# Kernel tuning notes

Hardware: AMD Instinct MI355X
Metric: run time of the kernel (lower is better)

## Reference

```python
import jax, jax.numpy as jnp
import numpy as np

D = 100  # input_size


def _gru_scan(x, h0, wi, wh, bi, bh):
    # x: [B,T,Din], h0: [B,H], wi: [3H,Din], wh: [3H,H]  (PyTorch r,z,n gate order)
    xw = jnp.einsum('btd,gd->btg', x, wi) + bi  # [B,T,3H]
    def step(h, xt):
        gh = h @ wh.T + bh
        xr, xz, xn = jnp.split(xt, 3, axis=-1)
        hr, hz, hn = jnp.split(gh, 3, axis=-1)
        r = jax.nn.sigmoid(xr + hr)
        z = jax.nn.sigmoid(xz + hz)
        n = jnp.tanh(xn + r * hn)
        hn2 = (1 - z) * n + z * h
        return hn2, hn2
    _, ys = jax.lax.scan(step, h0, jnp.swapaxes(xw, 0, 1))
    return jnp.swapaxes(ys, 0, 1)  # [B,T,H]


def _bigru(x, wi, wh, bi, bh):
    B = x.shape[0]
    H = wh.shape[-1]
    h0 = jnp.zeros((B, H), x.dtype)
    f = _gru_scan(x, h0, wi[0], wh[0], bi[0], bh[0])
    b = _gru_scan(x[:, ::-1], h0, wi[1], wh[1], bi[1], bh[1])[:, ::-1]
    return jnp.concatenate([f, b], axis=-1)


def _gru_cell(x, h, wi, wh, bi, bh):
    gx = x @ wi.T + bi
    gh = h @ wh.T + bh
    xr, xz, xn = jnp.split(gx, 3, axis=-1)
    hr, hz, hn = jnp.split(gh, 3, axis=-1)
    r = jax.nn.sigmoid(xr + hr)
    z = jax.nn.sigmoid(xz + hz)
    n = jnp.tanh(xn + r * hn)
    return (1 - z) * n + z * h


def setup_inputs() -> dict:
    key = jax.random.key(0)
    ks = iter(jax.random.split(key, 40))
    def n(shape, s=0.08):
        return (jax.random.normal(next(ks), shape) * s).astype(jnp.float32)
    B, T, L, V = 32, 512, 64, 400000
    inp = {
        'x_word': jax.random.randint(next(ks), (B, T), 0, V),
        'x_query': jax.random.randint(next(ks), (B, L), 0, V),
        'embed': n((V, D), 0.3),
        'ctx_wi': n((2, 3 * D, D)), 'ctx_wh': n((2, 3 * D, D)),
        'ctx_bi': n((2, 3 * D)), 'ctx_bh': n((2, 3 * D)),
        'mod0_wi': n((2, 3 * D, 8 * D)), 'mod0_wh': n((2, 3 * D, D)),
        'mod0_bi': n((2, 3 * D)), 'mod0_bh': n((2, 3 * D)),
        'mod1_wi': n((2, 3 * D, 2 * D)), 'mod1_wh': n((2, 3 * D, D)),
        'mod1_bi': n((2, 3 * D)), 'mod1_bh': n((2, 3 * D)),
        'w_sim': n((6 * D,)),
        'enc_wi': n((12 * D, 2 * D)), 'enc_wh': n((12 * D, 4 * D)),
        'enc_bi': n((12 * D,)), 'enc_bh': n((12 * D,)),
        'dec_wi': n((12 * D, 2 * D)), 'dec_wh': n((12 * D, 4 * D)),
        'dec_bi': n((12 * D,)), 'dec_bh': n((12 * D,)),
        'w1': n((2 * D, 4 * D)), 'w2': n((2 * D, 4 * D)), 'vt': n((2 * D,)),
    }
    return inp


def reference(x_word, x_query, embed, ctx_wi, ctx_wh, ctx_bi, ctx_bh,
              mod0_wi, mod0_wh, mod0_bi, mod0_bh, mod1_wi, mod1_wh, mod1_bi, mod1_bh,
              w_sim, enc_wi, enc_wh, enc_bi, enc_bh, dec_wi, dec_wh, dec_bi, dec_bh,
              w1, w2, vt):
    B, T = x_word.shape
    # shared bidirectional context encoder over both context and query
    h = _bigru(embed[x_word], ctx_wi, ctx_wh, ctx_bi, ctx_bh)   # [B,T,2D]
    u = _bigru(embed[x_query], ctx_wi, ctx_wh, ctx_bi, ctx_bh)  # [B,L,2D]
    # trilinear similarity W @ cat(h,u,h*u), fused (no [B,T,L,6D] materialization)
    w1s, w2s, w3s = jnp.split(w_sim, 3)
    S = (jnp.einsum('btd,d->bt', h, w1s)[:, :, None]
         + jnp.einsum('bld,d->bl', u, w2s)[:, None, :]
         + jnp.einsum('btd,bld->btl', h * w3s, u))               # [B,T,L]
    c2q = jnp.einsum('btl,bld->btd', jax.nn.softmax(S, axis=-1), u)
    b_att = jax.nn.softmax(jnp.max(S, axis=2), axis=-1)          # [B,T]
    q2c = jnp.einsum('bt,btd->bd', b_att, h)[:, None, :]         # [B,1,2D]
    G = jnp.concatenate([h, c2q, h * c2q, h * q2c], axis=-1)     # [B,T,8D]
    # 2-layer bidirectional modeling GRU
    M = _bigru(G, mod0_wi, mod0_wh, mod0_bi, mod0_bh)
    M = _bigru(M, mod1_wi, mod1_wh, mod1_bi, mod1_bh)            # [B,T,2D]
    # pointer network
    enc = _gru_scan(M, jnp.zeros((B, 4 * D), M.dtype), enc_wi, enc_wh, enc_bi, enc_bh)  # [B,T,4D]
    enc_w1 = jnp.einsum('bth,ph->btp', enc, w1)                  # precompute W1 @ enc
    hid = jnp.zeros((B, 4 * D), M.dtype)
    dec_in = jnp.zeros((B, 2 * D), M.dtype)  # never updated (as in original)
    probs = []
    for _ in range(2):  # answers = 2 (start, end)
        hid = _gru_cell(dec_in, hid, dec_wi, dec_wh, dec_bi, dec_bh)
        blend = jnp.tanh(enc_w1 + (hid @ w2.T)[:, None, :])      # [B,T,2D]
        out = jnp.einsum('btp,p->bt', blend, vt)
        probs.append(jax.nn.log_softmax(out, axis=-1))
    return jnp.stack(probs, axis=1)  # [B,2,T]
```

## Files before the change

### kernel.cpp

```cpp
#include <hip/hip_runtime.h>
#include <hip/hip_bf16.h>

typedef __hip_bfloat16 bf16;
typedef unsigned long long u64;
typedef __attribute__((ext_vector_type(8))) short s8v;
typedef __attribute__((ext_vector_type(4))) short s4v;
typedef __attribute__((ext_vector_type(4))) float f4v;

#define DEV __device__ __forceinline__

DEV float to_f32(float x) { return x; }
DEV float to_f32(bf16 x) { return __bfloat162float(x); }
DEV void store_c(float* p, float v) { *p = v; }
DEV void store_c(bf16* p, float v) { *p = __float2bfloat16(v); }
DEV float sigmf(float x) { return 1.f / (1.f + __expf(-x)); }
DEV short f2bs(float x) { bf16 h = __float2bfloat16(x); return *(short*)&h; }

__global__ void cvt_all(const float* __restrict__ s0, bf16* __restrict__ d0,
                        const float* __restrict__ s1, bf16* __restrict__ d1,
                        const float* __restrict__ s2, bf16* __restrict__ d2,
                        const float* __restrict__ s3, bf16* __restrict__ d3,
                        const float* __restrict__ s4, bf16* __restrict__ d4) {
  int i = blockIdx.x * blockDim.x + threadIdx.x;
  if (i < 60000) d0[i] = __float2bfloat16(s0[i]);
  i -= 60000;
  if (i >= 0 && i < 480000) d1[i] = __float2bfloat16(s1[i]);
  i -= 480000;
  if (i >= 0 && i < 120000) d2[i] = __float2bfloat16(s2[i]);
  i -= 120000;
  if (i >= 0 && i < 240000) d3[i] = __float2bfloat16(s3[i]);
  i -= 240000;
  if (i >= 0 && i < 80000) d4[i] = __float2bfloat16(s4[i]);
}

template <typename TC, bool HAS_BIAS, bool GATHER>
__global__ __launch_bounds__(256) void gemm_mfma(
    const bf16* __restrict__ A, const int* __restrict__ idx,
    const float* __restrict__ embedp, const bf16* __restrict__ W,
    const float* __restrict__ bias, TC* __restrict__ C,
    int M, int N, int K) {
  __shared__ short Als[128 * 32];
  __shared__ short Wls[128 * 32];
  const int tid = threadIdx.x;
  const int m0 = blockIdx.x * 128;
  const int n0 = blockIdx.y * 128;
  const int lane = tid & 63;
  const int wv = tid >> 6;
  const int wm = wv >> 1, wn = wv & 1;
  const int lq = lane >> 4, lr = lane & 15;
  const int row2 = tid >> 1;
  const int half = tid & 1;

  int vrow = 0;
  if (GATHER) vrow = idx[m0 + row2];
  const int nrow = n0 + row2;

  f4v acc[4][4];
#pragma unroll
  for (int i = 0; i < 4; ++i)
#pragma unroll
    for (int j = 0; j < 4; ++j) acc[i][j] = (f4v){0.f, 0.f, 0.f, 0.f};

  for (int k0 = 0; k0 < K; k0 += 32) {
#pragma unroll
    for (int ss = 0; ss < 4; ++ss) {
      int kk = k0 + half * 16 + ss * 4;
      short* dst = &Als[row2 * 32 + half * 16 + ss * 4];
      if (GATHER) {
        if (kk + 4 <= K) {
          float4 a4 = *(const float4*)(embedp + (size_t)vrow * 100 + kk);
          s4v v = {f2bs(a4.x), f2bs(a4.y), f2bs(a4.z), f2bs(a4.w)};
          *(s4v*)dst = v;
        } else {
#pragma unroll
          for (int j = 0; j < 4; ++j)
            dst[j] = (kk + j < K) ? f2bs(embedp[(size_t)vrow * 100 + kk + j]) : (short)0;
        }
      } else {
        const short* src = (const short*)(A + (size_t)(m0 + row2) * K + kk);
        if (kk + 4 <= K) {
          *(s4v*)dst = *(const s4v*)src;
        } else {
#pragma unroll
          for (int j = 0; j < 4; ++j) dst[j] = (kk + j < K) ? src[j] : (short)0;
        }
      }
    }
#pragma unroll
    for (int ss = 0; ss < 4; ++ss) {
      int kk = k0 + half * 16 + ss * 4;
      short* dst = &Wls[row2 * 32 + half * 16 + ss * 4];
      if (nrow < N) {
        const short* src = (const short*)(W + (size_t)nrow * K + kk);
        if (kk + 4 <= K) {
          *(s4v*)dst = *(const s4v*)src;
        } else {
#pragma unroll
          for (int j = 0; j < 4; ++j) dst[j] = (kk + j < K) ? src[j] : (short)0;
        }
      } else {
        *(s4v*)dst = (s4v){0, 0, 0, 0};
      }
    }
    __syncthreads();
    s8v af[4], bfr[4];
#pragma unroll
    for (int mi = 0; mi < 4; ++mi) {
      int r = wm * 64 + mi * 16 + lr;
      af[mi] = *(const s8v*)&Als[r * 32 + lq * 8];
    }
#pragma unroll
    for (int ni = 0; ni < 4; ++ni) {
      int r = wn * 64 + ni * 16 + lr;
      bfr[ni] = *(const s8v*)&Wls[r * 32 + lq * 8];
    }
#pragma unroll
    for (int mi = 0; mi < 4; ++mi)
#pragma unroll
      for (int ni = 0; ni < 4; ++ni)
        acc[mi][ni] = __builtin_amdgcn_mfma_f32_16x16x32_bf16(af[mi], bfr[ni], acc[mi][ni], 0, 0, 0);
    __syncthreads();
  }
#pragma unroll
  for (int mi = 0; mi < 4; ++mi) {
#pragma unroll
    for (int ni = 0; ni < 4; ++ni) {
      int n = n0 + wn * 64 + ni * 16 + lr;
      if (n >= N) continue;
      float bv = HAS_BIAS ? bias[n] : 0.f;
#pragma unroll
      for (int r = 0; r < 4; ++r) {
        int m = m0 + wm * 64 + mi * 16 + lq * 4 + r;
        store_c(&C[(size_t)m * N + n], acc[mi][ni][r] + bv);
      }
    }
  }
}

template <typename TO>
__global__ __launch_bounds__(192) void gru_scan100_dual(
    const bf16* __restrict__ xw0, const bf16* __restrict__ xw1,
    const float* __restrict__ wh,
    const float* __restrict__ bh,
    TO* __restrict__ out0, TO* __restrict__ out1,
    int T0, int T1) {
  const int b = blockIdx.x;
  const int y = blockIdx.y;
  const int which = y >> 1, dir = y & 1;
  const bf16* xw = which ? xw1 : xw0;
  TO* out = which ? out1 : out0;
  const int T = which ? T1 : T0;
  __shared__ float h_s[100];
  __shared__ float g_s[300];
  const int tid = threadIdx.x;
  float w0[100], w1[100];
  float bias0 = 0.f, bias1 = 0.f;
  if (tid < 150) {
    const float* wr0 = wh + (size_t)dir * 30000 + (size_t)(2 * tid) * 100;
#pragma unroll
    for (int c = 0; c < 25; ++c) {
      float4 v = *(const float4*)(wr0 + 4 * c);
      w0[4 * c] = v.x; w0[4 * c + 1] = v.y; w0[4 * c + 2] = v.z; w0[4 * c + 3] = v.w;
      float4 u = *(const float4*)(wr0 + 100 + 4 * c);
      w1[4 * c] = u.x; w1[4 * c + 1] = u.y; w1[4 * c + 2] = u.z; w1[4 * c + 3] = u.w;
    }
    bias0 = bh[dir * 300 + 2 * tid];
    bias1 = bh[dir * 300 + 2 * tid + 1];
  }
  if (tid < 100) h_s[tid] = 0.f;
  float pxr = 0.f, pxz = 0.f, pxn = 0.f;
  if (tid < 100) {
    int t0 = dir ? (T - 1) : 0;
    size_t base = ((size_t)b * T + t0) * 600 + dir * 300;
    pxr = to_f32(xw[base + tid]);
    pxz = to_f32(xw[base + 100 + tid]);
    pxn = to_f32(xw[base + 200 + tid]);
  }
  __syncthreads();
  for (int step = 0; step < T; ++step) {
    int t = dir ? (T - 1 - step) : step;
    if (tid < 150) {
      float a0 = bias0, a1 = 0.f, a2 = 0.f, a3 = 0.f;
      float b0 = bias1, b1 = 0.f, b2 = 0.f, b3 = 0.f;
#pragma unroll
      for (int c = 0; c < 25; ++c) {
        float4 h4 = *(const float4*)(&h_s[4 * c]);
        a0 += w0[4 * c] * h4.x; a1 += w0[4 * c + 1] * h4.y;
        a2 += w0[4 * c + 2] * h4.z; a3 += w0[4 * c + 3] * h4.w;
        b0 += w1[4 * c] * h4.x; b1 += w1[4 * c + 1] * h4.y;
        b2 += w1[4 * c + 2] * h4.z; b3 += w1[4 * c + 3] * h4.w;
      }
      g_s[2 * tid] = (a0 + a1) + (a2 + a3);
      g_s[2 * tid + 1] = (b0 + b1) + (b2 + b3);
    }
    __syncthreads();
    if (tid < 100) {
      float rr = sigmf(pxr + g_s[tid]);
      float zz = sigmf(pxz + g_s[100 + tid]);
      float nn = tanhf(pxn + rr * g_s[200 + tid]);
      float hn = (1.f - zz) * nn + zz * h_s[tid];
      h_s[tid] = hn;
      store_c(&out[((size_t)b * T + t) * 200 + dir * 100 + tid], hn);
      if (step + 1 < T) {
        int tn = dir ? (T - 2 - step) : (step + 1);
        size_t basen = ((size_t)b * T + tn) * 600 + dir * 300;
        pxr = to_f32(xw[basen + tid]);
        pxz = to_f32(xw[basen + 100 + tid]);
        pxn = to_f32(xw[basen + 200 + tid]);
      }
    }
    __syncthreads();
  }
}

__global__ __launch_bounds__(640) void gru_scan_enc_tag(
    const bf16* __restrict__ xw,
    const float* __restrict__ wh,
    const float* __restrict__ bh,
    bf16* __restrict__ out,
    u64* __restrict__ hx,
    int T) {
  const int b = blockIdx.x, s = blockIdx.y;
  __shared__ float h_s[400];
  __shared__ float g_s[150];
  const int tid = threadIdx.x;
  const int g = tid >> 2, p = tid & 3;
  const bool active = (tid < 600);
  float w[100];
  float bias = 0.f;
  if (active) {
    int i = g % 50, grp = g / 50;
    int gidx = grp * 400 + s * 50 + i;
    const float* wrow = wh + (size_t)gidx * 400 + p * 100;
#pragma unroll
    for (int c = 0; c < 25; ++c) {
      float4 v = *(const float4*)(wrow + 4 * c);
      w[4 * c] = v.x; w[4 * c + 1] = v.y; w[4 * c + 2] = v.z; w[4 * c + 3] = v.w;
    }
    if (p == 0) bias = bh[gidx];
  }
  for (int k = tid; k < 400; k += 640) h_s[k] = 0.f;
  const int myi = s * 50 + tid;
  float pxr = 0.f, pxz = 0.f, pxn = 0.f;
  if (tid < 50) {
    size_t base0 = (size_t)b * T * 1200;
    pxr = to_f32(xw[base0 + myi]);
    pxz = to_f32(xw[base0 + 400 + myi]);
    pxn = to_f32(xw[base0 + 800 + myi]);
  }
  __syncthreads();

  for (int t = 0; t < T; ++t) {
    if (active) {
      const int hb = p * 100;
      float4 hbuf[25];
#pragma unroll
      for (int c = 0; c < 25; ++c) hbuf[c] = *(const float4*)(&h_s[hb + 4 * c]);
      float a0 = bias, a1 = 0.f, a2 = 0.f, a3 = 0.f;
#pragma unroll
      for (int c = 0; c < 25; ++c) {
        a0 += w[4 * c] * hbuf[c].x; a1 += w[4 * c + 1] * hbuf[c].y;
        a2 += w[4 * c + 2] * hbuf[c].z; a3 += w[4 * c + 3] * hbuf[c].w;
      }
      float acc = (a0 + a1) + (a2 + a3);
      acc += __shfl_xor(acc, 1);
      acc += __shfl_xor(acc, 2);
      if (p == 0) g_s[g] = acc;
    }
    __syncthreads();
    const int par = (t + 1) & 1;
    u64* hxp = hx + ((size_t)b * 2 + par) * 400;
    if (tid < 50) {
      float rr = sigmf(pxr + g_s[tid]);
      float zz = sigmf(pxz + g_s[50 + tid]);
      float nn = tanhf(pxn + rr * g_s[100 + tid]);
      float hn = (1.f - zz) * nn + zz * h_s[myi];
      out[((size_t)b * T + t) * 400 + myi] = __float2bfloat16(hn);
      h_s[myi] = hn;
      u64 pack = (u64)__float_as_uint(hn) | ((u64)(unsigned)(t + 1) << 32);
      __hip_atomic_store(&hxp[myi], pack, __ATOMIC_RELAXED, __HIP_MEMORY_SCOPE_AGENT);
      if (t + 1 < T) {
        size_t basen = ((size_t)b * T + (t + 1)) * 1200;
        pxr = to_f32(xw[basen + myi]);
        pxz = to_f32(xw[basen + 400 + myi]);
        pxn = to_f32(xw[basen + 800 + myi]);
      }
    }
    if (tid < 400 && (tid / 50) != s) {
      const u64* src = &hxp[tid];
      u64 v;
      for (;;) {
        v = __hip_atomic_load(src, __ATOMIC_RELAXED, __HIP_MEMORY_SCOPE_AGENT);
        if ((unsigned)(v >> 32) == (unsigned)(t + 1)) break;
        __builtin_amdgcn_s_sleep(1);
      }
      h_s[tid] = __uint_as_float((unsigned)v);
    }
    __syncthreads();
  }
}

__global__ __launch_bounds__(256) void attn_main(
    const float* __restrict__ h, const float* __restrict__ u,
    const float* __restrict__ w_sim, float* __restrict__ c2q,
    float* __restrict__ smax, int T) {
  const int b = blockIdx.x;
  const int t0 = blockIdx.y * 32;
  __shared__ float u_s[64 * 201];
  __shared__ float w1_s[200], w2_s[200], w3_s[200];
  __shared__ float th_s[32], tu_s[64];
  __shared__ float hw3_s[200];
  __shared__ float Sp[4][64];
  __shared__ float A_s[64];
  const int tid = threadIdx.x;
  for (int i = tid; i < 64 * 200; i += 256) {
    int l = i / 200, d = i - l * 200;
    u_s[l * 201 + d] = u[((size_t)b * 64 + l) * 200 + d];
  }
  if (tid < 200) {
    w1_s[tid] = w_sim[tid];
    w2_s[tid] = w_sim[200 + tid];
    w3_s[tid] = w_sim[400 + tid];
  }
  __syncthreads();
  {
    int r = tid >> 2, sg = tid & 3;
    float p = 0.f;
    for (int j = 0; j < 50; ++j) p += u_s[r * 201 + sg * 50 + j] * w2_s[sg * 50 + j];
    p += __shfl_down(p, 2);
    p += __shfl_down(p, 1);
    if (sg == 0) tu_s[r] = p;
  }
  {
    int r = tid >> 3, sg = tid & 7;
    float p = 0.f;
    const float* hr = h + ((size_t)b * T + t0 + r) * 200 + sg * 25;
    for (int j = 0; j < 25; ++j) p += hr[j] * w1_s[sg * 25 + j];
    p += __shfl_down(p, 4);
    p += __shfl_down(p, 2);
    p += __shfl_down(p, 1);
    if (sg == 0) th_s[r] = p;
  }
  __syncthreads();
  for (int tt = 0; tt < 32; ++tt) {
    int t = t0 + tt;
    if (tid < 200) hw3_s[tid] = h[((size_t)b * T + t) * 200 + tid] * w3_s[tid];
    __syncthreads();
    int l = tid & 63, q = tid >> 6;
    float p = 0.f;
    for (int d = q * 50; d < q * 50 + 50; ++d) p += hw3_s[d] * u_s[l * 201 + d];
    Sp[q][l] = p;
    __syncthreads();
    if (tid < 64) {
      float s = th_s[tt] + tu_s[l] + Sp[0][l] + Sp[1][l] + Sp[2][l] + Sp[3][l];
      float m = s;
      for (int off = 32; off; off >>= 1) m = fmaxf(m, __shfl_xor(m, off));
      float e = __expf(s - m);
      float ssum = e;
      for (int off = 32; off; off >>= 1) ssum += __shfl_xor(ssum, off);
      A_s[l] = e / ssum;
      if (l == 0) smax[b * T + t] = m;
    }
    __syncthreads();
    if (tid < 200) {
      float acc = 0.f;
      for (int l2 = 0; l2 < 64; ++l2) acc += A_s[l2] * u_s[l2 * 201 + tid];
      c2q[((size_t)b * T + t) * 200 + tid] = acc;
    }
    __syncthreads();
  }
}

__global__ __launch_bounds__(256) void softmax_q2c(
    const float* __restrict__ smaxv, const float* __restrict__ h,
    float* __restrict__ q2c, int T) {
  int b = blockIdx.x;
  int tid = threadIdx.x;
  __shared__ float red[256];
  __shared__ float batt_s[512];
  float m = -1e30f;
  for (int t = tid; t < T; t += 256) m = fmaxf(m, smaxv[b * T + t]);
  red[tid] = m;
  __syncthreads();
  for (int s = 128; s; s >>= 1) {
    if (tid < s) red[tid] = fmaxf(red[tid], red[tid + s]);
    __syncthreads();
  }
  m = red[0];
  __syncthreads();
  float sum = 0.f;
  for (int t = tid; t < T; t += 256) {
    float e = __expf(smaxv[b * T + t] - m);
    batt_s[t] = e;
    sum += e;
  }
  red[tid] = sum;
  __syncthreads();
  for (int s = 128; s; s >>= 1) {
    if (tid < s) red[tid] += red[tid + s];
    __syncthreads();
  }
  float inv = 1.f / red[0];
  __syncthreads();
  if (tid < 200) {
    float acc = 0.f;
    for (int t = 0; t < T; ++t) acc += batt_s[t] * h[((size_t)b * T + t) * 200 + tid];
    q2c[b * 200 + tid] = acc * inv;
  }
}

__global__ void build_G(const float* __restrict__ h, const float* __restrict__ c2q,
                        const float* __restrict__ q2c, bf16* __restrict__ G, int T) {
  size_t i = (size_t)blockIdx.x * blockDim.x + threadIdx.x;
  if (i >= (size_t)32 * T * 200) return;
  size_t row = i / 200;
  int d = (int)(i - row * 200);
  int b = (int)(row / T);
  float hv = h[i];
  float cv = c2q[i];
  float qv = q2c[b * 200 + d];
  bf16* g = G + row * 800;
  g[d] = __float2bfloat16(hv);
  g[200 + d] = __float2bfloat16(cv);
  g[400 + d] = __float2bfloat16(hv * cv);
  g[600 + d] = __float2bfloat16(hv * qv);
}

__global__ __launch_bounds__(512) void decoder_small(
    const float* __restrict__ dwh, const float* __restrict__ dbi,
    const float* __restrict__ dbh, const float* __restrict__ w2,
    float* __restrict__ d2out) {
  __shared__ float hid[400];
  __shared__ float hid2[400];
  __shared__ float gh[1200];
  const int tid = threadIdx.x;
  if (tid < 400) {
    float r = sigmf(dbi[tid] + dbh[tid]);
    float z = sigmf(dbi[400 + tid] + dbh[400 + tid]);
    float n = tanhf(dbi[800 + tid] + r * dbh[800 + tid]);
    hid[tid] = (1.f - z) * n;
  }
  __syncthreads();
  if (tid < 200) {
    float a = 0.f;
    for (int k = 0; k < 400; ++k) a += w2[(size_t)tid * 400 + k] * hid[k];
    d2out[tid] = a;
  }
  for (int j = tid; j < 1200; j += 512) {
    float a = dbh[j];
    for (int k = 0; k < 400; ++k) a += dwh[(size_t)j * 400 + k] * hid[k];
    gh[j] = a;
  }
  __syncthreads();
  if (tid < 400) {
    float r = sigmf(dbi[tid] + gh[tid]);
    float z = sigmf(dbi[400 + tid] + gh[400 + tid]);
    float n = tanhf(dbi[800 + tid] + r * gh[800 + tid]);
    hid2[tid] = (1.f - z) * n + z * hid[tid];
  }
  __syncthreads();
  if (tid < 200) {
    float a = 0.f;
    for (int k = 0; k < 400; ++k) a += w2[(size_t)tid * 400 + k] * hid2[k];
    d2out[200 + tid] = a;
  }
}

__global__ __launch_bounds__(512) void logits_lsm(
    const float* __restrict__ encw1, const float* __restrict__ d2,
    const float* __restrict__ vt, float* __restrict__ outp, int T) {
  int b = blockIdx.x;
  __shared__ float lg[2][512];
  __shared__ float red[512];
  const int tid = threadIdx.x;
  const int wave = tid >> 6, lane = tid & 63;
  for (int r = wave; r < T; r += 8) {
    const float* e = encw1 + ((size_t)b * T + r) * 200;
    float s0 = 0.f, s1 = 0.f;
    for (int p = lane; p < 200; p += 64) {
      float ev = e[p], v = vt[p];
      s0 += tanhf(ev + d2[p]) * v;
      s1 += tanhf(ev + d2[200 + p]) * v;
    }
    for (int off = 32; off; off >>= 1) {
      s0 += __shfl_down(s0, off);
      s1 += __shfl_down(s1, off);
    }
    if (lane == 0) { lg[0][r] = s0; lg[1][r] = s1; }
  }
  __syncthreads();
  for (int it = 0; it < 2; ++it) {
    red[tid] = lg[it][tid];
    __syncthreads();
    for (int s = 256; s; s >>= 1) {
      if (tid < s) red[tid] = fmaxf(red[tid], red[tid + s]);
      __syncthreads();
    }
    float m = red[0];
    __syncthreads();
    red[tid] = __expf(lg[it][tid] - m);
    __syncthreads();
    for (int s = 256; s; s >>= 1) {
      if (tid < s) red[tid] += red[tid + s];
      __syncthreads();
    }
    float lse = m + __logf(red[0]);
    __syncthreads();
    outp[((size_t)b * 2 + it) * T + tid] = lg[it][tid] - lse;
  }
}

extern "C" void kernel_launch(void* const* d_in, const int* in_sizes, int n_in,
                              void* d_out, int out_size, void* d_ws, size_t ws_size,
                              hipStream_t stream) {
  (void)in_sizes; (void)n_in; (void)out_size; (void)ws_size;
  const int B = 32, T = 512, L = 64;
  const int BT = B * T;
  const int BL = B * L;

  const int* x_word = (const int*)d_in[0];
  const int* x_query = (const int*)d_in[1];
  const float* embed = (const float*)d_in[2];
  const float* ctx_wi = (const float*)d_in[3];
  const float* ctx_wh = (const float*)d_in[4];
  const float* ctx_bi = (const float*)d_in[5];
  const float* ctx_bh = (const float*)d_in[6];
  const float* mod0_wi = (const float*)d_in[7];
  const float* mod0_wh = (const float*)d_in[8];
  const float* mod0_bi = (const float*)d_in[9];
  const float* mod0_bh = (const float*)d_in[10];
  const float* mod1_wi = (const float*)d_in[11];
  const float* mod1_wh = (const float*)d_in[12];
  const float* mod1_bi = (const float*)d_in[13];
  const float* mod1_bh = (const float*)d_in[14];
  const float* w_sim = (const float*)d_in[15];
  const float* enc_wi = (const float*)d_in[16];
  const float* enc_wh = (const float*)d_in[17];
  const float* enc_bi = (const float*)d_in[18];
  const float* enc_bh = (const float*)d_in[19];
  const float* dec_wh = (const float*)d_in[21];
  const float* dec_bi = (const float*)d_in[22];
  const float* dec_bh = (const float*)d_in[23];
  const float* w1 = (const float*)d_in[24];
  const float* w2 = (const float*)d_in[25];
  const float* vt = (const float*)d_in[26];
  float* out_f = (float*)d_out;

  char* ws = (char*)d_ws;
  size_t off = 0;
  auto alloc = [&](size_t bytes) -> void* {
    void* p = ws + off;
    off += (bytes + 255) & ~(size_t)255;
    return p;
  };
  u64* hx = (u64*)alloc((size_t)B * 2 * 400 * 8);
  bf16* ctx_wibf = (bf16*)alloc((size_t)60000 * 2);
  bf16* mod0_wibf = (bf16*)alloc((size_t)480000 * 2);
  bf16* mod1_wibf = (bf16*)alloc((size_t)120000 * 2);
  bf16* enc_wibf = (bf16*)alloc((size_t)240000 * 2);
  bf16* w1bf = (bf16*)alloc((size_t)80000 * 2);
  char* RA = (char*)alloc((size_t)BT * 1200 * 2);
  bf16* xwFB = (bf16*)RA;
  bf16* xwe = (bf16*)RA;
  bf16* xwq = (bf16*)alloc((size_t)BL * 600 * 2);
  char* RB = (char*)alloc((size_t)BT * 800 * 2);
  bf16* G = (bf16*)RB;
  bf16* enc_outbf = (bf16*)RB;
  char* RC = (char*)alloc((size_t)2 * BT * 200 * 4);
  float* h_cat = (float*)RC;
  float* c2q = (float*)(RC + (size_t)BT * 200 * 4);
  bf16* M0bf = (bf16*)c2q;
  bf16* Mxbf = (bf16*)h_cat;
  float* encw1 = c2q;
  float* u_cat = (float*)alloc((size_t)BL * 200 * 4);
  float* smaxb = (float*)alloc((size_t)BT * 4);
  float* q2cb = (float*)alloc((size_t)B * 200 * 4);
  float* d2 = (float*)alloc((size_t)400 * 4);

  hipMemsetAsync(hx, 0, (size_t)B * 2 * 400 * 8, stream);

  cvt_all<<<(980000 + 255) / 256, 256, 0, stream>>>(ctx_wi, ctx_wibf, mod0_wi, mod0_wibf,
                                                    mod1_wi, mod1_wibf, enc_wi, enc_wibf,
                                                    w1, w1bf);

  gemm_mfma<bf16, true, true><<<dim3(BT / 128, 5), 256, 0, stream>>>(
      nullptr, x_word, embed, ctx_wibf, ctx_bi, xwFB, BT, 600, 100);
  gemm_mfma<bf16, true, true><<<dim3(BL / 128, 5), 256, 0, stream>>>(
      nullptr, x_query, embed, ctx_wibf, ctx_bi, xwq, BL, 600, 100);

  gru_scan100_dual<float><<<dim3(B, 4), 192, 0, stream>>>(
      xwFB, xwq, ctx_wh, ctx_bh, h_cat, u_cat, T, L);

  attn_main<<<dim3(B, T / 32), 256, 0, stream>>>(h_cat, u_cat, w_sim, c2q, smaxb, T);
  softmax_q2c<<<B, 256, 0, stream>>>(smaxb, h_cat, q2cb, T);
  build_G<<<(BT * 200 + 255) / 256, 256, 0, stream>>>(h_cat, c2q, q2cb, G, T);

  gemm_mfma<bf16, true, false><<<dim3(BT / 128, 5), 256, 0, stream>>>(
      G, nullptr, nullptr, mod0_wibf, mod0_bi, xwFB, BT, 600, 800);
  gru_scan100_dual<bf16><<<dim3(B, 2), 192, 0, stream>>>(
      xwFB, nullptr, mod0_wh, mod0_bh, M0bf, nullptr, T, T);

  gemm_mfma<bf16, true, false><<<dim3(BT / 128, 5), 256, 0, stream>>>(
      M0bf, nullptr, nullptr, mod1_wibf, mod1_bi, xwFB, BT, 600, 200);
  gru_scan100_dual<bf16><<<dim3(B, 2), 192, 0, stream>>>(
      xwFB, nullptr, mod1_wh, mod1_bh, Mxbf, nullptr, T, T);

  gemm_mfma<bf16, true, false><<<dim3(BT / 128, 10), 256, 0, stream>>>(
      Mxbf, nullptr, nullptr, enc_wibf, enc_bi, xwe, BT, 1200, 200);
  gru_scan_enc_tag<<<dim3(B, 8), 640, 0, stream>>>(xwe, enc_wh, enc_bh, enc_outbf, hx, T);
  gemm_mfma<float, false, false><<<dim3(BT / 128, 2), 256, 0, stream>>>(
      enc_outbf, nullptr, nullptr, w1bf, nullptr, encw1, BT, 200, 400);

  decoder_small<<<1, 512, 0, stream>>>(dec_wh, dec_bi, dec_bh, w2, d2);
  logits_lsm<<<B, 512, 0, stream>>>(encw1, d2, vt, out_f, T);
}
```

Baseline: 3.192 ms.

## Double-buffer LDS tiles in MFMA GEMM with register prefetch

The bf16 MFMA GEMM now prefetches the next K-tile of A and W into registers while the current tile is computed, then writes it to a second LDS buffer. This removes one barrier per K-step and overlaps global-load latency with the MFMA work. It costs twice the LDS and extra registers, which may lower occupancy. The GEMMs are probably a small share of a total dominated by the sequential GRU scans.

```diff
diff --git a/kernel.cpp b/kernel.cpp
--- a/kernel.cpp
+++ b/kernel.cpp
@@ -39,8 +39,8 @@
     const float* __restrict__ embedp, const bf16* __restrict__ W,
     const float* __restrict__ bias, TC* __restrict__ C,
     int M, int N, int K) {
-  __shared__ short Als[128 * 32];
-  __shared__ short Wls[128 * 32];
+  __shared__ short Als[2][128 * 32];
+  __shared__ short Wls[2][128 * 32];
   const int tid = threadIdx.x;
   const int m0 = blockIdx.x * 128;
   const int n0 = blockIdx.y * 128;
@@ -55,71 +55,90 @@
   if (GATHER) vrow = idx[m0 + row2];
   const int nrow = n0 + row2;
 
-  f4v acc[4][4];
-#pragma unroll
-  for (int i = 0; i < 4; ++i)
-#pragma unroll
-    for (int j = 0; j < 4; ++j) acc[i][j] = (f4v){0.f, 0.f, 0.f, 0.f};
-
-  for (int k0 = 0; k0 < K; k0 += 32) {
+  s4v ra[4], rw[4];
+  auto load_regs = [&](int k0) {
 #pragma unroll
     for (int ss = 0; ss < 4; ++ss) {
       int kk = k0 + half * 16 + ss * 4;
-      short* dst = &Als[row2 * 32 + half * 16 + ss * 4];
       if (GATHER) {
         if (kk + 4 <= K) {
           float4 a4 = *(const float4*)(embedp + (size_t)vrow * 100 + kk);
-          s4v v = {f2bs(a4.x), f2bs(a4.y), f2bs(a4.z), f2bs(a4.w)};
-          *(s4v*)dst = v;
+          ra[ss] = (s4v){f2bs(a4.x), f2bs(a4.y), f2bs(a4.z), f2bs(a4.w)};
         } else {
+          s4v v = {0, 0, 0, 0};
 #pragma unroll
           for (int j = 0; j < 4; ++j)
-            dst[j] = (kk + j < K) ? f2bs(embedp[(size_t)vrow * 100 + kk + j]) : (short)0;
+            if (kk + j < K) v[j] = f2bs(embedp[(size_t)vrow * 100 + kk + j]);
+          ra[ss] = v;
         }
       } else {
         const short* src = (const short*)(A + (size_t)(m0 + row2) * K + kk);
         if (kk + 4 <= K) {
-          *(s4v*)dst = *(const s4v*)src;
+          ra[ss] = *(const s4v*)src;
         } else {
-#pragma unroll
-          for (int j = 0; j < 4; ++j) dst[j] = (kk + j < K) ? src[j] : (short)0;
+          s4v v = {0, 0, 0, 0};
+#pragma unroll
+          for (int j = 0; j < 4; ++j)
+            if (kk + j < K) v[j] = src[j];
+          ra[ss] = v;
         }
       }
-    }
-#pragma unroll
-    for (int ss = 0; ss < 4; ++ss) {
-      int kk = k0 + half * 16 + ss * 4;
-      short* dst = &Wls[row2 * 32 + half * 16 + ss * 4];
       if (nrow < N) {
         const short* src = (const short*)(W + (size_t)nrow * K + kk);
         if (kk + 4 <= K) {
-          *(s4v*)dst = *(const s4v*)src;
+          rw[ss] = *(const s4v*)src;
         } else {
-#pragma unroll
-          for (int j = 0; j < 4; ++j) dst[j] = (kk + j < K) ? src[j] : (short)0;
+          s4v v = {0, 0, 0, 0};
+#pragma unroll
+          for (int j = 0; j < 4; ++j)
+            if (kk + j < K) v[j] = src[j];
+          rw[ss] = v;
         }
       } else {
-        *(s4v*)dst = (s4v){0, 0, 0, 0};
-      }
-    }
-    __syncthreads();
+        rw[ss] = (s4v){0, 0, 0, 0};
+      }
+    }
+  };
+  auto write_lds = [&](int buf) {
+#pragma unroll
+    for (int ss = 0; ss < 4; ++ss) {
+      *(s4v*)&Als[buf][row2 * 32 + half * 16 + ss * 4] = ra[ss];
+      *(s4v*)&Wls[buf][row2 * 32 + half * 16 + ss * 4] = rw[ss];
+    }
+  };
+
+  f4v acc[4][4];
+#pragma unroll
+  for (int i = 0; i < 4; ++i)
+#pragma unroll
+    for (int j = 0; j < 4; ++j) acc[i][j] = (f4v){0.f, 0.f, 0.f, 0.f};
+
+  const int nk = (K + 31) / 32;
+  load_regs(0);
+  write_lds(0);
+  __syncthreads();
+  int cur = 0;
+  for (int ki = 0; ki < nk; ++ki) {
+    if (ki + 1 < nk) load_regs((ki + 1) * 32);
     s8v af[4], bfr[4];
 #pragma unroll
     for (int mi = 0; mi < 4; ++mi) {
       int r = wm * 64 + mi * 16 + lr;
-      af[mi] = *(const s8v*)&Als[r * 32 + lq * 8];
+      af[mi] = *(const s8v*)&Als[cur][r * 32 + lq * 8];
     }
 #pragma unroll
     for (int ni = 0; ni < 4; ++ni) {
       int r = wn * 64 + ni * 16 + lr;
-      bfr[ni] = *(const s8v*)&Wls[r * 32 + lq * 8];
+      bfr[ni] = *(const s8v*)&Wls[cur][r * 32 + lq * 8];
     }
 #pragma unroll
     for (int mi = 0; mi < 4; ++mi)
 #pragma unroll
       for (int ni = 0; ni < 4; ++ni)
         acc[mi][ni] = __builtin_amdgcn_mfma_f32_16x16x32_bf16(af[mi], bfr[ni], acc[mi][ni], 0, 0, 0);
-    __syncthreads();
+    if (ki + 1 < nk) write_lds(cur ^ 1);
+    __syncthreads();
+    cur ^= 1;
   }
 #pragma unroll
   for (int mi = 0; mi < 4; ++mi) {
```

Result: no change. 3.185 ms (-0.2%).
